# Kernel tuning notes

Measured on AMD Instinct MI355X. Metric: run time of the kernel, lower is better.

The kernel has to match this reference:

```python
import jax, jax.numpy as jnp
import numpy as np

E, B, D, H, NH, GH = 8, 16384, 1024, 512, 8, 128
DH = H // NH


def setup_inputs() -> dict:
    key = jax.random.key(0)
    ks = jax.random.split(key, 16)
    w = lambda i, shape: jax.random.normal(ks[i], shape, jnp.float32) * 0.02
    return dict(
        freq_feats=jax.random.normal(ks[0], (E, B, D), jnp.float32),
        sem_feat=jax.random.normal(ks[1], (B, D), jnp.float32),
        # query_proj (shared across experts)
        Wq=w(2, (D, H)), bq=jnp.zeros((H,), jnp.float32),
        # per-expert key/value input projections (stacked)
        Wk=w(3, (E, D, H)), bk=jnp.zeros((E, H), jnp.float32),
        Wv=w(4, (E, D, H)), bv=jnp.zeros((E, H), jnp.float32),
        # per-expert MultiheadAttention in_proj (q/k/v splits) and out_proj
        Wqm=w(5, (E, H, H)), bqm=jnp.zeros((E, H), jnp.float32),
        Wkm=w(6, (E, H, H)), bkm=jnp.zeros((E, H), jnp.float32),
        Wvm=w(7, (E, H, H)), bvm=jnp.zeros((E, H), jnp.float32),
        Wo=w(8, (E, H, H)), bo=jnp.zeros((E, H), jnp.float32),
        # gate network: Linear(D,GH) -> ReLU -> Linear(GH,E)
        Wg1=w(9, (D, GH)), bg1=jnp.zeros((GH,), jnp.float32),
        Wg2=w(10, (GH, E)), bg2=jnp.zeros((E,), jnp.float32),
    )


def reference(freq_feats, sem_feat, Wq, bq, Wk, bk, Wv, bv,
              Wqm, bqm, Wkm, bkm, Wvm, bvm, Wo, bo,
              Wg1, bg1, Wg2, bg2):
    # shared query projection: (B, H)
    q = sem_feat @ Wq + bq
    # stacked per-expert key/value projections: (E, B, H)
    K = jnp.einsum('ebd,edh->ebh', freq_feats, Wk) + bk[:, None, :]
    V = jnp.einsum('ebd,edh->ebh', freq_feats, Wv) + bv[:, None, :]
    # MultiheadAttention in-projections (seq_len = 1 for q, k, v)
    qm = jnp.einsum('bh,ehg->ebg', q, Wqm) + bqm[:, None, :]  # (E, B, H)
    km = jnp.einsum('ebh,ehg->ebg', K, Wkm) + bkm[:, None, :]
    vm = jnp.einsum('ebh,ehg->ebg', V, Wvm) + bvm[:, None, :]
    qh = qm.reshape(E, B, NH, DH)
    kh = km.reshape(E, B, NH, DH)
    vh = vm.reshape(E, B, NH, DH)
    # single key/value -> scores (E, B, NH, 1); softmax over 1 key == 1
    scores = jnp.sum(qh * kh, axis=-1, keepdims=True) / jnp.sqrt(jnp.float32(DH))
    attn_w = jax.nn.softmax(scores, axis=-1)  # all-ones (degenerate softmax)
    ctx = (attn_w * vh).reshape(E, B, H)
    expert_out = jnp.einsum('ebh,ehg->ebg', ctx, Wo) + bo[:, None, :]  # (E, B, H)
    # semantic-conditioned meta-gate: (B, E)
    gate_logits = jax.nn.relu(sem_feat @ Wg1 + bg1) @ Wg2 + bg2
    gate = jax.nn.softmax(gate_logits, axis=-1)
    # gate-weighted sum over experts: (B, H)
    fused = jnp.einsum('ebh,be->bh', expert_out, gate)
    return fused
```

## Files before the change

kernel.cpp:

```cpp
#include <hip/hip_runtime.h>

#define B_  16384
#define D_  1024
#define H_  512
#define E_  8
#define GH_ 128

typedef __fp16 h2  __attribute__((ext_vector_type(2)));
typedef __fp16 h8  __attribute__((ext_vector_type(8)));
typedef float  f4v __attribute__((ext_vector_type(4)));

#define BM  128
#define BN  128
#define BK  32
#define LDP 40

union HU { h2 h[4]; h8 v; };

__device__ __forceinline__ unsigned asu(h2 x) { return __builtin_bit_cast(unsigned, x); }

template<int MODE, bool RB>
__global__ __launch_bounds__(256, 3)
void gemm_pre(const float* __restrict__ A, long sA, int lda,
              const float* __restrict__ Bm, long sB, int ldb, int K,
              float* __restrict__ Cf, long sC, int ldc,
              const float* __restrict__ bias,
              __fp16* __restrict__ Ct, int ldt, int mStride)
{
    __shared__ __fp16 As[BM * LDP];
    __shared__ __fp16 Bs[BN * LDP];
    const int t    = threadIdx.x;
    const int bm0  = blockIdx.x * BM;
    const int n0   = blockIdx.y * BN;
    const int e    = blockIdx.z;
    A  += (long)e * sA;
    Bm += (long)e * sB;

    const int lane = t & 63, w = t >> 6, quad = lane >> 4, l16 = lane & 15;
    const int wrow = w & 1, wcol = w >> 1;

    const int arow = t >> 1, ach = t & 1;
    const float* aSrc = A + (long)(bm0 + arow) * lda + ach * 16;
    __fp16* aDst = &As[arow * LDP + ach * 16];

    const int kb = t >> 5, nb = t & 31;
    const float* bSrc = Bm + (long)(kb * 4) * ldb + n0 + nb * 4;
    __fp16* bDst = &Bs[(nb * 4) * LDP + kb * 4];

    f4v acc[4][4] = {};

    const int ksteps = K / BK;
    for (int ks = 0; ks < ksteps; ++ks) {
        const float* ap = aSrc + ks * BK;
        f4v a0 = *(const f4v*)(ap);
        f4v a1 = *(const f4v*)(ap + 4);
        f4v a2 = *(const f4v*)(ap + 8);
        f4v a3 = *(const f4v*)(ap + 12);
        const float* bp = bSrc + (long)ks * BK * ldb;
        f4v r0 = *(const f4v*)(bp);
        f4v r1 = *(const f4v*)(bp + ldb);
        f4v r2 = *(const f4v*)(bp + 2 * ldb);
        f4v r3 = *(const f4v*)(bp + 3 * ldb);

        __syncthreads();

        HU u0, u1;
        u0.h[0] = __builtin_amdgcn_cvt_pkrtz(a0.x, a0.y);
        u0.h[1] = __builtin_amdgcn_cvt_pkrtz(a0.z, a0.w);
        u0.h[2] = __builtin_amdgcn_cvt_pkrtz(a1.x, a1.y);
        u0.h[3] = __builtin_amdgcn_cvt_pkrtz(a1.z, a1.w);
        u1.h[0] = __builtin_amdgcn_cvt_pkrtz(a2.x, a2.y);
        u1.h[1] = __builtin_amdgcn_cvt_pkrtz(a2.z, a2.w);
        u1.h[2] = __builtin_amdgcn_cvt_pkrtz(a3.x, a3.y);
        u1.h[3] = __builtin_amdgcn_cvt_pkrtz(a3.z, a3.w);
        *(h8*)aDst       = u0.v;
        *(h8*)(aDst + 8) = u1.v;

        h2 P0 = __builtin_amdgcn_cvt_pkrtz(r0.x, r0.y);
        h2 P1 = __builtin_amdgcn_cvt_pkrtz(r1.x, r1.y);
        h2 P2 = __builtin_amdgcn_cvt_pkrtz(r2.x, r2.y);
        h2 P3 = __builtin_amdgcn_cvt_pkrtz(r3.x, r3.y);
        h2 Q0 = __builtin_amdgcn_cvt_pkrtz(r0.z, r0.w);
        h2 Q1 = __builtin_amdgcn_cvt_pkrtz(r1.z, r1.w);
        h2 Q2 = __builtin_amdgcn_cvt_pkrtz(r2.z, r2.w);
        h2 Q3 = __builtin_amdgcn_cvt_pkrtz(r3.z, r3.w);
        uint2 c0 = make_uint2(__builtin_amdgcn_perm(asu(P1), asu(P0), 0x05040100),
                              __builtin_amdgcn_perm(asu(P3), asu(P2), 0x05040100));
        uint2 c1 = make_uint2(__builtin_amdgcn_perm(asu(P1), asu(P0), 0x07060302),
                              __builtin_amdgcn_perm(asu(P3), asu(P2), 0x07060302));
        uint2 c2 = make_uint2(__builtin_amdgcn_perm(asu(Q1), asu(Q0), 0x05040100),
                              __builtin_amdgcn_perm(asu(Q3), asu(Q2), 0x05040100));
        uint2 c3 = make_uint2(__builtin_amdgcn_perm(asu(Q1), asu(Q0), 0x07060302),
                              __builtin_amdgcn_perm(asu(Q3), asu(Q2), 0x07060302));
        *(uint2*)(bDst)           = c0;
        *(uint2*)(bDst + LDP)     = c1;
        *(uint2*)(bDst + 2 * LDP) = c2;
        *(uint2*)(bDst + 3 * LDP) = c3;

        __syncthreads();

        h8 af[4], bf[4];
        #pragma unroll
        for (int i = 0; i < 4; ++i)
            af[i] = *(const h8*)&As[(wrow * 64 + i * 16 + l16) * LDP + quad * 8];
        #pragma unroll
        for (int j = 0; j < 4; ++j)
            bf[j] = *(const h8*)&Bs[(wcol * 64 + j * 16 + l16) * LDP + quad * 8];
        #pragma unroll
        for (int i = 0; i < 4; ++i) {
            #pragma unroll
            for (int j = 0; j < 4; ++j)
                acc[i][j] = __builtin_amdgcn_mfma_f32_16x16x32_f16(af[i], bf[j], acc[i][j], 0, 0, 0);
        }
    }

    if constexpr (MODE == 0) {
        float* C = Cf + (long)e * sC;
        #pragma unroll
        for (int j = 0; j < 4; ++j) {
            const int cg = n0 + wcol * 64 + j * 16 + l16;
            float bb = 0.f;
            if constexpr (RB) bb = bias[cg];
            #pragma unroll
            for (int i = 0; i < 4; ++i) {
                const int rb = bm0 + wrow * 64 + i * 16 + quad * 4;
                #pragma unroll
                for (int r = 0; r < 4; ++r) {
                    float v = acc[i][j][r] + bb;
                    if constexpr (RB) v = fmaxf(v, 0.f);
                    C[(long)(rb + r) * ldc + cg] = v;
                }
            }
        }
    } else {
        #pragma unroll
        for (int j = 0; j < 4; ++j) {
            const int n = n0 + wcol * 64 + j * 16 + l16;
            #pragma unroll
            for (int i = 0; i < 4; ++i) {
                const int m = e * mStride + bm0 + wrow * 64 + i * 16 + quad * 4;
                union { h2 hh[2]; uint2 u; } up;
                up.hh[0] = __builtin_amdgcn_cvt_pkrtz(acc[i][j][0], acc[i][j][1]);
                up.hh[1] = __builtin_amdgcn_cvt_pkrtz(acc[i][j][2], acc[i][j][3]);
                *(uint2*)&Ct[(long)n * ldt + m] = up.u;
            }
        }
    }
}

__global__ void k_bc(const float* __restrict__ bv, const float* __restrict__ bvm,
                     const float* __restrict__ bo, const float* __restrict__ Wo,
                     const float* __restrict__ VmO, float* __restrict__ bc)
{
    const int idx = blockIdx.x * 256 + threadIdx.x;
    const int e = idx >> 9, h = idx & 511;
    const float* vmo = VmO + (long)e * H_ * H_ + h;
    const float* wo  = Wo  + (long)e * H_ * H_ + h;
    const float* bve  = bv  + e * H_;
    const float* bvme = bvm + e * H_;
    float s = bo[e * H_ + h];
    for (int g = 0; g < H_; ++g)
        s += bve[g] * vmo[(long)g * H_] + bvme[g] * wo[(long)g * H_];
    bc[e * H_ + h] = s;
}

__global__ __launch_bounds__(256)
void k_gate(const float* __restrict__ H1, const float* __restrict__ Wg2,
            const float* __restrict__ bg2, float* __restrict__ gate)
{
    __shared__ float Wg2s[GH_ * E_];
    __shared__ float Lg[64][E_];
    const int t = threadIdx.x;
    *(f4v*)&Wg2s[t * 4] = *(const f4v*)&Wg2[t * 4];
    __syncthreads();

    const int r = t & 63, e2 = t >> 6;
    const int row = blockIdx.x * 64 + r;
    const int e0 = e2 * 2;
    const f4v* h4 = (const f4v*)(H1 + (long)row * GH_);
    float l0 = bg2[e0], l1 = bg2[e0 + 1];
    for (int g4 = 0; g4 < GH_ / 4; ++g4) {
        f4v hv = h4[g4];
        const int gb = g4 * 4 * E_;
        l0 += hv.x * Wg2s[gb + e0]      + hv.y * Wg2s[gb + 8 + e0]
            + hv.z * Wg2s[gb + 16 + e0] + hv.w * Wg2s[gb + 24 + e0];
        l1 += hv.x * Wg2s[gb + e0 + 1]      + hv.y * Wg2s[gb + 8 + e0 + 1]
            + hv.z * Wg2s[gb + 16 + e0 + 1] + hv.w * Wg2s[gb + 24 + e0 + 1];
    }
    Lg[r][e0] = l0; Lg[r][e0 + 1] = l1;
    __syncthreads();
    if (t < 64) {
        float m = Lg[t][0];
        #pragma unroll
        for (int e = 1; e < E_; ++e) m = fmaxf(m, Lg[t][e]);
        float ex[E_], s = 0.f;
        #pragma unroll
        for (int e = 0; e < E_; ++e) { ex[e] = __expf(Lg[t][e] - m); s += ex[e]; }
        const float inv = 1.f / s;
        float* gr = gate + (long)(blockIdx.x * 64 + t) * E_;
        #pragma unroll
        for (int e = 0; e < E_; ++e) gr[e] = ex[e] * inv;
    }
}

__global__ __launch_bounds__(256, 3)
void k_main(const float* __restrict__ freq, const float* __restrict__ gate,
            const __fp16* __restrict__ WcT, const float* __restrict__ bc,
            float* __restrict__ out)
{
    __shared__ __fp16 As[BM * LDP];
    __shared__ __fp16 Bs[BN * LDP];
    __shared__ float gateS[BM * E_];
    __shared__ float bcS[E_ * BN];

    const int t    = threadIdx.x;
    const int bm0  = blockIdx.x * BM;
    const int n0   = blockIdx.y * BN;
    const int lane = t & 63, w = t >> 6, quad = lane >> 4, l16 = lane & 15;
    const int wrow = w & 1, wcol = w >> 1;

    const int arow = t >> 1, ach = t & 1;
    const int brow = bm0 + arow;
    const float*  aBase = freq + (long)brow * D_ + ach * 16;
    const __fp16* wBase = WcT + (long)(n0 + arow) * (E_ * D_) + ach * 16;
    __fp16* aDst = &As[arow * LDP + ach * 16];
    __fp16* bDst = &Bs[arow * LDP + ach * 16];

    f4v acc[4][4] = {};
    h2 gh = {(__fp16)0, (__fp16)0};

    for (int ks = 0; ks < (E_ * D_) / BK; ++ks) {
        const int eb = ks >> 5;
        const float* ap = aBase + (long)eb * (B_ * D_) + (ks & 31) * BK;
        f4v a0 = *(const f4v*)(ap);
        f4v a1 = *(const f4v*)(ap + 4);
        f4v a2 = *(const f4v*)(ap + 8);
        f4v a3 = *(const f4v*)(ap + 12);
        const __fp16* wp = wBase + ks * BK;
        h8 w0 = *(const h8*)(wp);
        h8 w1 = *(const h8*)(wp + 8);
        if ((ks & 31) == 0) {
            const float g = gate[brow * E_ + eb];
            const __fp16 gs = (__fp16)g;
            gh = (h2){gs, gs};
        }

        __syncthreads();

        HU u0, u1;
        u0.h[0] = __builtin_amdgcn_cvt_pkrtz(a0.x, a0.y) * gh;
        u0.h[1] = __builtin_amdgcn_cvt_pkrtz(a0.z, a0.w) * gh;
        u0.h[2] = __builtin_amdgcn_cvt_pkrtz(a1.x, a1.y) * gh;
        u0.h[3] = __builtin_amdgcn_cvt_pkrtz(a1.z, a1.w) * gh;
        u1.h[0] = __builtin_amdgcn_cvt_pkrtz(a2.x, a2.y) * gh;
        u1.h[1] = __builtin_amdgcn_cvt_pkrtz(a2.z, a2.w) * gh;
        u1.h[2] = __builtin_amdgcn_cvt_pkrtz(a3.x, a3.y) * gh;
        u1.h[3] = __builtin_amdgcn_cvt_pkrtz(a3.z, a3.w) * gh;
        *(h8*)aDst       = u0.v;
        *(h8*)(aDst + 8) = u1.v;
        *(h8*)bDst       = w0;
        *(h8*)(bDst + 8) = w1;

        __syncthreads();

        h8 af[4], bf[4];
        #pragma unroll
        for (int i = 0; i < 4; ++i)
            af[i] = *(const h8*)&As[(wrow * 64 + i * 16 + l16) * LDP + quad * 8];
        #pragma unroll
        for (int j = 0; j < 4; ++j)
            bf[j] = *(const h8*)&Bs[(wcol * 64 + j * 16 + l16) * LDP + quad * 8];
        #pragma unroll
        for (int i = 0; i < 4; ++i) {
            #pragma unroll
            for (int j = 0; j < 4; ++j)
                acc[i][j] = __builtin_amdgcn_mfma_f32_16x16x32_f16(af[i], bf[j], acc[i][j], 0, 0, 0);
        }
    }

    *(f4v*)&gateS[t * 4] = *(const f4v*)&gate[(long)bm0 * E_ + t * 4];
    *(f4v*)&bcS[t * 4]   = *(const f4v*)&bc[(t >> 5) * H_ + n0 + (t & 31) * 4];
    __syncthreads();

    #pragma unroll
    for (int j = 0; j < 4; ++j) {
        const int cl = wcol * 64 + j * 16 + l16;
        float bv8[E_];
        #pragma unroll
        for (int e = 0; e < E_; ++e) bv8[e] = bcS[e * BN + cl];
        #pragma unroll
        for (int i = 0; i < 4; ++i) {
            const int rl = wrow * 64 + i * 16 + quad * 4;
            #pragma unroll
            for (int r = 0; r < 4; ++r) {
                const float* gr = &gateS[(rl + r) * E_];
                float bias = 0.f;
                #pragma unroll
                for (int e = 0; e < E_; ++e) bias += gr[e] * bv8[e];
                out[(long)(bm0 + rl + r) * H_ + (n0 + cl)] = acc[i][j][r] + bias;
            }
        }
    }
}

extern "C" void kernel_launch(void* const* d_in, const int* in_sizes, int n_in,
                              void* d_out, int out_size, void* d_ws, size_t ws_size,
                              hipStream_t stream)
{
    const float* freq = (const float*)d_in[0];
    const float* sem  = (const float*)d_in[1];
    const float* Wv   = (const float*)d_in[6];
    const float* bv   = (const float*)d_in[7];
    const float* Wvm  = (const float*)d_in[12];
    const float* bvm  = (const float*)d_in[13];
    const float* Wo   = (const float*)d_in[14];
    const float* bo   = (const float*)d_in[15];
    const float* Wg1  = (const float*)d_in[16];
    const float* bg1  = (const float*)d_in[17];
    const float* Wg2  = (const float*)d_in[18];
    const float* bg2  = (const float*)d_in[19];
    float* out = (float*)d_out;

    char* ws = (char*)d_ws;
    float*   VmO  = (float*)ws;
    __fp16*  WcT  = (__fp16*)(ws + (8l << 20));
    float*   bc   = (float*)(ws + (16l << 20));
    float*   H1   = (float*)(ws + (16l << 20) + (1l << 16));
    float*   gate = (float*)(ws + (24l << 20) + (1l << 16));

    gemm_pre<0, false><<<dim3(4, 4, 8), 256, 0, stream>>>(
        Wvm, (long)H_ * H_, H_, Wo, (long)H_ * H_, H_, H_,
        VmO, (long)H_ * H_, H_, nullptr, nullptr, 0, 0);

    k_bc<<<16, 256, 0, stream>>>(bv, bvm, bo, Wo, VmO, bc);

    gemm_pre<1, false><<<dim3(8, 4, 8), 256, 0, stream>>>(
        Wv, (long)D_ * H_, H_, VmO, (long)H_ * H_, H_, H_,
        nullptr, 0, 0, nullptr, WcT, E_ * D_, D_);

    gemm_pre<0, true><<<dim3(128, 1, 1), 256, 0, stream>>>(
        sem, 0, D_, Wg1, 0, GH_, D_,
        H1, 0, GH_, bg1, nullptr, 0, 0);

    k_gate<<<256, 256, 0, stream>>>(H1, Wg2, bg2, gate);

    k_main<<<dim3(128, 4), 256, 0, stream>>>(freq, gate, WcT, bc, out);
}
```

Measured before the change: 1.211 ms.

## Double-buffer LDS tiles and prefetch two K-steps ahead in main GEMM

The main fused GEMM loop now uses two LDS buffers for the A and B tiles and issues global loads for tiles k+2/k+3 while computing on the current buffer. This leaves one barrier per K-step instead of two and overlaps global-load latency with MFMA work. The barrier macro waits only on lgkmcnt, so pending global loads are not drained at the barrier. The cost is double the LDS footprint and more registers, and launch bounds drop from 3 to 2 blocks per SM, which lowers occupancy.

```diff
diff --git a/kernel.cpp b/kernel.cpp
--- a/kernel.cpp
+++ b/kernel.cpp
@@ -203,13 +203,66 @@
     }
 }
 
-__global__ __launch_bounds__(256, 3)
+
+#define SYNC() asm volatile("s_waitcnt lgkmcnt(0)\ns_barrier" ::: "memory")
+
+#define ISSUE(k, aR, wR) do {                                                  \
+    const int e_ = (k) >> 5;                                                   \
+    const float* ap_ = aBase + (long)e_ * ((long)B_ * D_) + ((k) & 31) * BK;   \
+    aR[0] = *(const f4v*)(ap_);                                                \
+    aR[1] = *(const f4v*)(ap_ + 4);                                            \
+    aR[2] = *(const f4v*)(ap_ + 8);                                            \
+    aR[3] = *(const f4v*)(ap_ + 12);                                           \
+    const __fp16* wp_ = wBase + (long)(k) * BK;                                \
+    wR[0] = *(const h8*)(wp_);                                                 \
+    wR[1] = *(const h8*)(wp_ + 8);                                             \
+} while (0)
+
+#define STAGE(half, aR, wR, gvv) do {                                          \
+    const __fp16 gs_ = (__fp16)(gvv);                                          \
+    const h2 gh_ = {gs_, gs_};                                                 \
+    HU u0_, u1_;                                                               \
+    u0_.h[0] = __builtin_amdgcn_cvt_pkrtz(aR[0].x, aR[0].y) * gh_;             \
+    u0_.h[1] = __builtin_amdgcn_cvt_pkrtz(aR[0].z, aR[0].w) * gh_;             \
+    u0_.h[2] = __builtin_amdgcn_cvt_pkrtz(aR[1].x, aR[1].y) * gh_;             \
+    u0_.h[3] = __builtin_amdgcn_cvt_pkrtz(aR[1].z, aR[1].w) * gh_;             \
+    u1_.h[0] = __builtin_amdgcn_cvt_pkrtz(aR[2].x, aR[2].y) * gh_;             \
+    u1_.h[1] = __builtin_amdgcn_cvt_pkrtz(aR[2].z, aR[2].w) * gh_;             \
+    u1_.h[2] = __builtin_amdgcn_cvt_pkrtz(aR[3].x, aR[3].y) * gh_;             \
+    u1_.h[3] = __builtin_amdgcn_cvt_pkrtz(aR[3].z, aR[3].w) * gh_;             \
+    __fp16* ad_ = aDst + (half) * (BM * LDP);                                  \
+    *(h8*)ad_       = u0_.v;                                                   \
+    *(h8*)(ad_ + 8) = u1_.v;                                                   \
+    __fp16* bd_ = bDst + (half) * (BM * LDP);                                  \
+    *(h8*)bd_       = wR[0];                                                   \
+    *(h8*)(bd_ + 8) = wR[1];                                                   \
+} while (0)
+
+#define COMPUTE(half) do {                                                     \
+    const __fp16* As_ = As + (half) * (BM * LDP);                              \
+    const __fp16* Bs_ = Bs + (half) * (BM * LDP);                              \
+    h8 af[4], bf[4];                                                           \
+    _Pragma("unroll")                                                          \
+    for (int i = 0; i < 4; ++i)                                                \
+        af[i] = *(const h8*)&As_[(wrow * 64 + i * 16 + l16) * LDP + quad * 8]; \
+    _Pragma("unroll")                                                          \
+    for (int j = 0; j < 4; ++j)                                                \
+        bf[j] = *(const h8*)&Bs_[(wcol * 64 + j * 16 + l16) * LDP + quad * 8]; \
+    _Pragma("unroll")                                                          \
+    for (int i = 0; i < 4; ++i) {                                              \
+        _Pragma("unroll")                                                      \
+        for (int j = 0; j < 4; ++j)                                            \
+            acc[i][j] = __builtin_amdgcn_mfma_f32_16x16x32_f16(af[i], bf[j], acc[i][j], 0, 0, 0); \
+    }                                                                          \
+} while (0)
+
+__global__ __launch_bounds__(256, 2)
 void k_main(const float* __restrict__ freq, const float* __restrict__ gate,
             const __fp16* __restrict__ WcT, const float* __restrict__ bc,
             float* __restrict__ out)
 {
-    __shared__ __fp16 As[BM * LDP];
-    __shared__ __fp16 Bs[BN * LDP];
+    __shared__ __fp16 As[2 * BM * LDP];
+    __shared__ __fp16 Bs[2 * BM * LDP];
     __shared__ float gateS[BM * E_];
     __shared__ float bcS[E_ * BN];
 
@@ -227,55 +280,38 @@
     __fp16* bDst = &Bs[arow * LDP + ach * 16];
 
     f4v acc[4][4] = {};
-    h2 gh = {(__fp16)0, (__fp16)0};
-
-    for (int ks = 0; ks < (E_ * D_) / BK; ++ks) {
-        const int eb = ks >> 5;
-        const float* ap = aBase + (long)eb * (B_ * D_) + (ks & 31) * BK;
-        f4v a0 = *(const f4v*)(ap);
-        f4v a1 = *(const f4v*)(ap + 4);
-        f4v a2 = *(const f4v*)(ap + 8);
-        f4v a3 = *(const f4v*)(ap + 12);
-        const __fp16* wp = wBase + ks * BK;
-        h8 w0 = *(const h8*)(wp);
-        h8 w1 = *(const h8*)(wp + 8);
-        if ((ks & 31) == 0) {
-            const float g = gate[brow * E_ + eb];
-            const __fp16 gs = (__fp16)g;
-            gh = (h2){gs, gs};
-        }
-
-        __syncthreads();
-
-        HU u0, u1;
-        u0.h[0] = __builtin_amdgcn_cvt_pkrtz(a0.x, a0.y) * gh;
-        u0.h[1] = __builtin_amdgcn_cvt_pkrtz(a0.z, a0.w) * gh;
-        u0.h[2] = __builtin_amdgcn_cvt_pkrtz(a1.x, a1.y) * gh;
-        u0.h[3] = __builtin_amdgcn_cvt_pkrtz(a1.z, a1.w) * gh;
-        u1.h[0] = __builtin_amdgcn_cvt_pkrtz(a2.x, a2.y) * gh;
-        u1.h[1] = __builtin_amdgcn_cvt_pkrtz(a2.z, a2.w) * gh;
-        u1.h[2] = __builtin_amdgcn_cvt_pkrtz(a3.x, a3.y) * gh;
-        u1.h[3] = __builtin_amdgcn_cvt_pkrtz(a3.z, a3.w) * gh;
-        *(h8*)aDst       = u0.v;
-        *(h8*)(aDst + 8) = u1.v;
-        *(h8*)bDst       = w0;
-        *(h8*)(bDst + 8) = w1;
-
-        __syncthreads();
-
-        h8 af[4], bf[4];
-        #pragma unroll
-        for (int i = 0; i < 4; ++i)
-            af[i] = *(const h8*)&As[(wrow * 64 + i * 16 + l16) * LDP + quad * 8];
-        #pragma unroll
-        for (int j = 0; j < 4; ++j)
-            bf[j] = *(const h8*)&Bs[(wcol * 64 + j * 16 + l16) * LDP + quad * 8];
-        #pragma unroll
-        for (int i = 0; i < 4; ++i) {
-            #pragma unroll
-            for (int j = 0; j < 4; ++j)
-                acc[i][j] = __builtin_amdgcn_mfma_f32_16x16x32_f16(af[i], bf[j], acc[i][j], 0, 0, 0);
-        }
+
+    const int NK = (E_ * D_) / BK;
+
+    f4v aE[4], aO[4];
+    h8  wE[2], wO[2];
+
+    ISSUE(0, aE, wE);
+    ISSUE(1, aO, wO);
+    float gv    = gate[brow * E_ + 0];
+    float gNext = 0.f;
+    STAGE(0, aE, wE, gv);
+    SYNC();
+
+    for (int ks = 0; ks < NK; ks += 2) {
+        if (ks + 2 < NK) {
+            ISSUE(ks + 2, aE, wE);
+            if (((ks + 2) & 31) == 0)
+                gNext = gate[brow * E_ + ((ks + 2) >> 5)];
+        }
+        COMPUTE(0);
+        STAGE(1, aO, wO, gv);
+        SYNC();
+
+        if (ks + 3 < NK) {
+            ISSUE(ks + 3, aO, wO);
+        }
+        COMPUTE(1);
+        if (ks + 2 < NK) {
+            if (((ks + 2) & 31) == 0) gv = gNext;
+            STAGE(0, aE, wE, gv);
+        }
+        SYNC();
     }
 
     *(f4v*)&gateS[t * 4] = *(const f4v*)&gate[(long)bm0 * E_ + t * 4];
```

New measurement: 1.210 ms. About the same (-0.0%).
